# Kernel optimization log

Hardware: AMD Instinct MI355X
Metric: run time of the kernel (lower is better)

## Reference

```python
import jax, jax.numpy as jnp
import numpy as np

D_MODEL = 32
N_HEADS = 8
QUERY_SHAPE = 24
MEM_FLANGE = 8


def conv2d(x, w, padding=1):
    return jax.lax.conv_general_dilated(
        x, w, window_strides=(1, 1),
        padding=[(padding, padding), (padding, padding)],
        dimension_numbers=('NCHW', 'OIHW', 'NCHW'))


def setup_inputs() -> dict:
    key = jax.random.key(0)
    k1, k2, k3, k4 = jax.random.split(key, 4)
    x = jax.random.normal(k1, (2, 32, 32, 480), dtype=jnp.float32)
    qkv_w = jax.random.normal(k2, (96, 32, 3, 3), dtype=jnp.float32) * 0.05
    qkv_b = jax.random.normal(k3, (96,), dtype=jnp.float32) * 0.05
    out_w = jax.random.normal(k4, (32, 32, 3, 3), dtype=jnp.float32) * 0.05
    return {'x': x, 'qkv_w': qkv_w, 'qkv_b': qkv_b, 'out_w': out_w}


def reference(x, qkv_w, qkv_b, out_w):
    qs, mf, nh = QUERY_SHAPE, MEM_FLANGE, N_HEADS
    dh = D_MODEL // nh  # depth per head

    qkv = conv2d(x, qkv_w) + qkv_b[None, :, None, None]  # [B, 3*d_model, H, W0]
    # pad time (last dim) to multiple of query_shape
    W0 = qkv.shape[-1]
    off = (-W0) % qs
    if off > 0:
        qkv = jnp.pad(qkv, ((0, 0), (0, 0), (0, 0), (0, off)))
    B, _, H, W = qkv.shape

    qkv = qkv.reshape(B, nh, 3 * dh, H, W)
    q, k, v = jnp.split(qkv, 3, axis=2)  # each [B, nh, dh, H, W]
    q = q * dh ** (-0.5)
    k = jnp.pad(k, ((0, 0),) * 4 + ((mf, mf),))
    v = jnp.pad(v, ((0, 0),) * 4 + ((mf, mf),))

    nb = W // qs            # number of time blocks
    wlen = qs + 2 * mf      # key window length
    # overlapping window gather indices: [nb, wlen]
    idx = jnp.arange(nb)[:, None] * qs + jnp.arange(wlen)[None, :]

    qb = q.reshape(B, nh, dh, H, nb, qs)      # [B,nh,dh,H,nb,qs]
    kb = k[..., idx]                          # [B,nh,dh,H,nb,wlen]
    vb = v[..., idx]                          # [B,nh,dh,H,nb,wlen]

    # flatten to per-block matmuls, matching torch permutes/reshapes
    qm = qb.transpose(0, 1, 4, 3, 5, 2).reshape(-1, H * qs, dh)        # [BN, H*qs, dh]
    km = kb.transpose(0, 1, 4, 2, 3, 5).reshape(-1, dh, H * wlen)      # [BN, dh, H*wlen]
    vm = vb.transpose(0, 1, 4, 3, 5, 2).reshape(-1, H * wlen, dh)      # [BN, H*wlen, dh]

    bias = (jnp.abs(km).sum(axis=-2, keepdims=True) == 0).astype(km.dtype) * (-1e-09)
    logits = qm @ km + bias                    # [BN, H*qs, H*wlen]
    weights = jax.nn.softmax(logits, axis=-1)
    out = weights @ vm                         # [BN, H*qs, dh]

    out = out.reshape(B, nh, nb, H, qs, dh)
    out = out.transpose(0, 1, 5, 3, 2, 4)      # [B, nh, dh, H, nb, qs]
    out = out.reshape(B, nh * dh, H, nb * qs)  # [B, d_model, H, W]
    out = out[..., :x.shape[2], :x.shape[3]]
    return conv2d(out, out_w)
```

## Files before the change

kernel.cpp:

```cpp
#include <hip/hip_runtime.h>
#include <hip/hip_bf16.h>


#define HW 15360
#define VSTRIDE 1300

typedef _Float16 half4 __attribute__((ext_vector_type(4)));
typedef float floatx4 __attribute__((ext_vector_type(4)));
using fh2 = decltype(__builtin_amdgcn_cvt_pkrtz(0.f, 0.f));

__global__ __launch_bounds__(256) void repack_gemm(
    const float* __restrict__ w1, uint2* __restrict__ wA1,
    const float* __restrict__ w2, uint2* __restrict__ wA2) {
    int i = blockIdx.x * 256 + threadIdx.x;
    const float* src; uint2* dst; int rel;
    if (i < 6 * 18 * 64)            { src = w1; dst = wA1; rel = i; }
    else if (i < (6 + 2) * 18 * 64) { src = w2; dst = wA2; rel = i - 6 * 18 * 64; }
    else return;
    int lane = rel & 63;
    int mk   = rel >> 6;
    int kt   = mk % 18;
    int m    = mk / 18;
    int co   = m * 16 + (lane & 15);
    int k0   = kt * 16 + (lane >> 4) * 4;
    float v[4];
#pragma unroll
    for (int j = 0; j < 4; ++j) {
        int k = k0 + j, tap = k >> 5, ci = k & 31;
        v[j] = src[co * 288 + ci * 9 + tap];
    }
    unsigned lo = __builtin_bit_cast(unsigned, __builtin_amdgcn_cvt_pkrtz(v[0], v[1]));
    unsigned hi = __builtin_bit_cast(unsigned, __builtin_amdgcn_cvt_pkrtz(v[2], v[3]));
    dst[mk * 64 + lane] = make_uint2(lo, hi);
}

__global__ __launch_bounds__(256) void conv1_gemm(
    const float* __restrict__ x, const uint2* __restrict__ wA,
    const float* __restrict__ bias, _Float16* __restrict__ qkv)
{
    __shared__ _Float16 S[6 * 18 * 36];

    int xb  = blockIdx.x;
    int byq = blockIdx.y;
    int mb  = blockIdx.z;
    int yq = byq & 7, b = byq >> 3;
    int y0 = yq * 4, x0 = xb * 16;
    int tid = threadIdx.x, lane = tid & 63, wv = tid >> 6;

    const float* xb_ = x + (size_t)b * 32 * HW;
    for (int e = tid; e < 3456; e += 256) {
        int col = e % 18; int t2 = e / 18; int row = t2 % 6; int ci = t2 / 6;
        int yg = y0 + row - 1, xg = x0 + col - 1;
        _Float16 v = (_Float16)0.f;
        if ((unsigned)yg < 32u && (unsigned)xg < 480u)
            v = (_Float16)xb_[ci * HW + yg * 480 + xg];
        S[(row * 18 + col) * 36 + ci] = v;
    }
    __syncthreads();

    int cb = lane & 15, kg = lane >> 4;

    half4 Bf[18];
#pragma unroll
    for (int kt = 0; kt < 18; ++kt) {
        int tap = kt >> 1;
        int dy = tap / 3, dx = tap % 3;
        int ci0 = (kt & 1) * 16 + kg * 4;
        Bf[kt] = *(const half4*)&S[((wv + dy) * 18 + cb + dx) * 36 + ci0];
    }

    floatx4 acc[3];
#pragma unroll
    for (int m = 0; m < 3; ++m) {
        const float4 bz = *(const float4*)&bias[(mb * 3 + m) * 16 + kg * 4];
        acc[m] = floatx4{ bz.x, bz.y, bz.z, bz.w };
    }

    for (int kt = 0; kt < 18; ++kt) {
        half4 bb = Bf[kt];
#pragma unroll
        for (int m = 0; m < 3; ++m) {
            uint2 aw = wA[((mb * 3 + m) * 18 + kt) * 64 + lane];
            acc[m] = __builtin_amdgcn_mfma_f32_16x16x16f16(
                __builtin_bit_cast(half4, aw), bb, acc[m], 0, 0, 0);
        }
    }

    size_t obase = (size_t)b * 96 * HW + (y0 + wv) * 480 + x0 + cb;
#pragma unroll
    for (int m = 0; m < 3; ++m)
#pragma unroll
        for (int r = 0; r < 4; ++r)
            qkv[obase + (size_t)((mb * 3 + m) * 16 + kg * 4 + r) * HW] =
                (_Float16)acc[m][r];
}

__global__ __launch_bounds__(256) void conv2_gemm(
    const _Float16* __restrict__ att, const uint2* __restrict__ wA,
    float* __restrict__ out)
{
    int xb  = blockIdx.x;
    int byq = blockIdx.y;
    int yq = byq & 7, b = byq >> 3;
    int y0 = yq * 4, x0 = xb * 16;
    int tid = threadIdx.x, lane = tid & 63, wv = tid >> 6;
    int cb = lane & 15, kg = lane >> 4;
    int yrow = y0 + wv;

    const _Float16* ab = att + (size_t)b * 15360 * 32;
    const half4 hz = { (_Float16)0.f, (_Float16)0.f, (_Float16)0.f, (_Float16)0.f };

    half4 Bf[18];
#pragma unroll
    for (int kt = 0; kt < 18; ++kt) {
        int tap = kt >> 1;
        int dy = tap / 3 - 1, dx = tap % 3 - 1;
        int ci0 = (kt & 1) * 16 + kg * 4;
        int yg = yrow + dy, xg = x0 + cb + dx;
        bool ok = ((unsigned)yg < 32u) & ((unsigned)xg < 480u);
        int yc = ok ? yg : 0, xc = ok ? xg : 0;
        half4 v = *(const half4*)&ab[((size_t)yc * 480 + xc) * 32 + ci0];
        Bf[kt] = ok ? v : hz;
    }

    floatx4 acc[2];
    acc[0] = floatx4{0.f, 0.f, 0.f, 0.f};
    acc[1] = floatx4{0.f, 0.f, 0.f, 0.f};

    for (int kt = 0; kt < 18; ++kt) {
        half4 bb = Bf[kt];
#pragma unroll
        for (int m = 0; m < 2; ++m) {
            uint2 aw = wA[(m * 18 + kt) * 64 + lane];
            acc[m] = __builtin_amdgcn_mfma_f32_16x16x16f16(
                __builtin_bit_cast(half4, aw), bb, acc[m], 0, 0, 0);
        }
    }

    size_t obase = (size_t)b * 32 * HW + yrow * 480 + x0 + cb;
#pragma unroll
    for (int m = 0; m < 2; ++m)
#pragma unroll
        for (int r = 0; r < 4; ++r)
            out[obase + (size_t)(m * 16 + kg * 4 + r) * HW] = acc[m][r];
}

__global__ __launch_bounds__(256) void attn_mfma(
    const _Float16* __restrict__ qkv, _Float16* __restrict__ att)
{
    __shared__ _Float16 Kl[1280 * 4];
    __shared__ _Float16 Vl[5 * VSTRIDE];
    __shared__ _Float16 Zl[8];

    int wg    = blockIdx.x;
    int orig  = (wg & 7) * 160 + (wg >> 3);
    int qg    = orig & 3;
    int bhblk = orig >> 2;
    int blk = bhblk % 20;
    int h   = (bhblk / 20) % 8;
    int b   = bhblk / 160;
    int tid  = threadIdx.x;
    int lane = tid & 63;
    int wv   = tid >> 6;

    const _Float16* base = qkv + (size_t)(b * 96 + h * 12) * HW;
    const _Float16* kb = base + 4 * HW;
    const _Float16* vb = base + 8 * HW;

    const _Float16 h0 = (_Float16)0.f;
    if (tid < 2) *(half4*)&Zl[tid * 4] = half4{ h0, h0, h0, h0 };

    for (int j = tid; j < 1280; j += 256) {
        int yy = j / 40, wc = j - yy * 40;
        int wpos = blk * 24 + wc - 8;
        _Float16 k0 = h0, k1 = h0, k2 = h0, k3 = h0;
        _Float16 v0 = h0, v1 = h0, v2 = h0, v3 = h0;
        if ((unsigned)wpos < 480u) {
            int o = yy * 480 + wpos;
            k0 = kb[o]; k1 = kb[o + HW]; k2 = kb[o + 2 * HW]; k3 = kb[o + 3 * HW];
            v0 = vb[o]; v1 = vb[o + HW]; v2 = vb[o + 2 * HW]; v3 = vb[o + 3 * HW];
        }
        *(half4*)&Kl[j * 4] = half4{ k0, k1, k2, k3 };
        Vl[j]               = v0;
        Vl[VSTRIDE + j]     = v1;
        Vl[2 * VSTRIDE + j] = v2;
        Vl[3 * VSTRIDE + j] = v3;
        Vl[4 * VSTRIDE + j] = (_Float16)1.0f;
    }

    const float QS = 0.5f * 1.44269504f;
    half4 qf[3];
#pragma unroll
    for (int t = 0; t < 3; ++t) {
        half4 qq = { h0, h0, h0, h0 };
        if (lane < 16) {
            int q = qg * 192 + (wv * 3 + t) * 16 + lane;
            int y = q / 24, qc = q - y * 24;
            int o = y * 480 + blk * 24 + qc;
            qq[0] = (_Float16)((float)base[o] * QS);
            qq[1] = (_Float16)((float)base[o + HW] * QS);
            qq[2] = (_Float16)((float)base[o + 2 * HW] * QS);
            qq[3] = (_Float16)((float)base[o + 3 * HW] * QS);
        }
        qf[t] = qq;
    }

    __syncthreads();

    const floatx4 fz = { 0.f, 0.f, 0.f, 0.f };
    floatx4 acc[3];
#pragma unroll
    for (int t = 0; t < 3; ++t) acc[t] = fz;

    int n = lane & 15;
    int g = lane >> 4;

    const _Float16* kap = (lane < 16) ? &Kl[n * 4] : Zl;
    int kstep = (lane < 16) ? 64 : 0;
    const _Float16* vap = (n <= 4) ? &Vl[n * VSTRIDE + g * 4] : Zl;
    int vstep = (n <= 4) ? 16 : 0;

    for (int kt = 0; kt < 80; ++kt) {
        half4 ka = *(const half4*)kap; kap += kstep;
        half4 vv = *(const half4*)vap; vap += vstep;
#pragma unroll
        for (int t = 0; t < 3; ++t) {
            floatx4 s = __builtin_amdgcn_mfma_f32_16x16x16f16(ka, qf[t], fz, 0, 0, 0);
            auto lo = __builtin_amdgcn_cvt_pkrtz(__builtin_amdgcn_exp2f(s[0]),
                                                 __builtin_amdgcn_exp2f(s[1]));
            auto hi = __builtin_amdgcn_cvt_pkrtz(__builtin_amdgcn_exp2f(s[2]),
                                                 __builtin_amdgcn_exp2f(s[3]));
            half4 pa = { (_Float16)lo[0], (_Float16)lo[1],
                         (_Float16)hi[0], (_Float16)hi[1] };
            acc[t] = __builtin_amdgcn_mfma_f32_16x16x16f16(pa, vv, acc[t], 0, 0, 0);
        }
    }

#pragma unroll
    for (int t = 0; t < 3; ++t) {
#pragma unroll
        for (int r = 0; r < 4; ++r) {
            float ls = __shfl(acc[t][r], (lane & 48) + 4);
            if (n < 4) {
                float val = acc[t][r] * __builtin_amdgcn_rcpf(ls);
                int q = qg * 192 + (wv * 3 + t) * 16 + g * 4 + r;
                int y = q / 24, qc = q - y * 24;
                att[((size_t)b * 15360 + y * 480 + blk * 24 + qc) * 32 + h * 4 + n] =
                    (_Float16)val;
            }
        }
    }
}

extern "C" void kernel_launch(void* const* d_in, const int* in_sizes, int n_in,
                              void* d_out, int out_size, void* d_ws, size_t ws_size,
                              hipStream_t stream) {
    const float* x     = (const float*)d_in[0];
    const float* qkv_w = (const float*)d_in[1];
    const float* qkv_b = (const float*)d_in[2];
    const float* out_w = (const float*)d_in[3];
    float* out = (float*)d_out;

    uint2* wA1 = (uint2*)d_ws;
    uint2* wA2 = wA1 + 6 * 18 * 64;
    _Float16* qkv16 = (_Float16*)(wA2 + 2 * 18 * 64);
    _Float16* att16 = qkv16 + (size_t)2 * 96 * HW;

    repack_gemm<<<(8 * 18 * 64 + 255) / 256, 256, 0, stream>>>(
        qkv_w, wA1, out_w, wA2);

    conv1_gemm<<<dim3(30, 16, 2), 256, 0, stream>>>(x, wA1, qkv_b, qkv16);

    attn_mfma<<<1280, 256, 0, stream>>>(qkv16, att16);

    conv2_gemm<<<dim3(30, 16), 256, 0, stream>>>(att16, wA2, out);
}
```

Before: 78.62 us.

## Store QKV intermediate channel-last so conv1 and attention use vector accesses

The fp16 QKV intermediate moves from a channel-planar layout [B,96,H,W] to a pixel-major, channel-last layout [B,H,W,96]. Conv1 now writes four adjacent channels with one half4 store instead of four scalar strided stores. The attention kernel loads each K, V and Q head slice as one 8-byte half4 per pixel instead of four scalar loads spaced HW apart. In exchange, neighbouring threads now access memory 192 bytes apart, which may coalesce less well than the old contiguous-per-channel accesses.

```diff
diff --git a/kernel.cpp b/kernel.cpp
--- a/kernel.cpp
+++ b/kernel.cpp
@@ -86,13 +86,13 @@
         }
     }
 
-    size_t obase = (size_t)b * 96 * HW + (y0 + wv) * 480 + x0 + cb;
-#pragma unroll
-    for (int m = 0; m < 3; ++m)
-#pragma unroll
-        for (int r = 0; r < 4; ++r)
-            qkv[obase + (size_t)((mb * 3 + m) * 16 + kg * 4 + r) * HW] =
-                (_Float16)acc[m][r];
+    size_t pbase = ((size_t)b * HW + (y0 + wv) * 480 + x0 + cb) * 96;
+#pragma unroll
+    for (int m = 0; m < 3; ++m) {
+        half4 hv = { (_Float16)acc[m][0], (_Float16)acc[m][1],
+                     (_Float16)acc[m][2], (_Float16)acc[m][3] };
+        *(half4*)&qkv[pbase + (mb * 3 + m) * 16 + kg * 4] = hv;
+    }
 }
 
 __global__ __launch_bounds__(256) void conv2_gemm(
@@ -107,7 +107,7 @@
     int cb = lane & 15, kg = lane >> 4;
     int yrow = y0 + wv;
 
-    const _Float16* ab = att + (size_t)b * 15360 * 32;
+    const _Float16* ab = att + (size_t)b * HW * 32;
     const half4 hz = { (_Float16)0.f, (_Float16)0.f, (_Float16)0.f, (_Float16)0.f };
 
     half4 Bf[18];
@@ -163,28 +163,26 @@
     int lane = tid & 63;
     int wv   = tid >> 6;
 
-    const _Float16* base = qkv + (size_t)(b * 96 + h * 12) * HW;
-    const _Float16* kb = base + 4 * HW;
-    const _Float16* vb = base + 8 * HW;
+    const _Float16* base = qkv + (size_t)b * HW * 96 + h * 12;
 
     const _Float16 h0 = (_Float16)0.f;
-    if (tid < 2) *(half4*)&Zl[tid * 4] = half4{ h0, h0, h0, h0 };
+    const half4 hz4 = { h0, h0, h0, h0 };
+    if (tid < 2) *(half4*)&Zl[tid * 4] = hz4;
 
     for (int j = tid; j < 1280; j += 256) {
         int yy = j / 40, wc = j - yy * 40;
         int wpos = blk * 24 + wc - 8;
-        _Float16 k0 = h0, k1 = h0, k2 = h0, k3 = h0;
-        _Float16 v0 = h0, v1 = h0, v2 = h0, v3 = h0;
+        half4 k4 = hz4, v4 = hz4;
         if ((unsigned)wpos < 480u) {
-            int o = yy * 480 + wpos;
-            k0 = kb[o]; k1 = kb[o + HW]; k2 = kb[o + 2 * HW]; k3 = kb[o + 3 * HW];
-            v0 = vb[o]; v1 = vb[o + HW]; v2 = vb[o + 2 * HW]; v3 = vb[o + 3 * HW];
-        }
-        *(half4*)&Kl[j * 4] = half4{ k0, k1, k2, k3 };
-        Vl[j]               = v0;
-        Vl[VSTRIDE + j]     = v1;
-        Vl[2 * VSTRIDE + j] = v2;
-        Vl[3 * VSTRIDE + j] = v3;
+            size_t o = (size_t)(yy * 480 + wpos) * 96;
+            k4 = *(const half4*)&base[o + 4];
+            v4 = *(const half4*)&base[o + 8];
+        }
+        *(half4*)&Kl[j * 4] = k4;
+        Vl[j]               = v4[0];
+        Vl[VSTRIDE + j]     = v4[1];
+        Vl[2 * VSTRIDE + j] = v4[2];
+        Vl[3 * VSTRIDE + j] = v4[3];
         Vl[4 * VSTRIDE + j] = (_Float16)1.0f;
     }
 
@@ -192,15 +190,16 @@
     half4 qf[3];
 #pragma unroll
     for (int t = 0; t < 3; ++t) {
-        half4 qq = { h0, h0, h0, h0 };
+        half4 qq = hz4;
         if (lane < 16) {
             int q = qg * 192 + (wv * 3 + t) * 16 + lane;
             int y = q / 24, qc = q - y * 24;
-            int o = y * 480 + blk * 24 + qc;
-            qq[0] = (_Float16)((float)base[o] * QS);
-            qq[1] = (_Float16)((float)base[o + HW] * QS);
-            qq[2] = (_Float16)((float)base[o + 2 * HW] * QS);
-            qq[3] = (_Float16)((float)base[o + 3 * HW] * QS);
+            size_t o = (size_t)(y * 480 + blk * 24 + qc) * 96;
+            half4 qv = *(const half4*)&base[o];
+            qq[0] = (_Float16)((float)qv[0] * QS);
+            qq[1] = (_Float16)((float)qv[1] * QS);
+            qq[2] = (_Float16)((float)qv[2] * QS);
+            qq[3] = (_Float16)((float)qv[3] * QS);
         }
         qf[t] = qq;
     }
@@ -245,7 +244,7 @@
                 float val = acc[t][r] * __builtin_amdgcn_rcpf(ls);
                 int q = qg * 192 + (wv * 3 + t) * 16 + g * 4 + r;
                 int y = q / 24, qc = q - y * 24;
-                att[((size_t)b * 15360 + y * 480 + blk * 24 + qc) * 32 + h * 4 + n] =
+                att[((size_t)b * HW + y * 480 + blk * 24 + qc) * 32 + h * 4 + n] =
                     (_Float16)val;
             }
         }
@@ -264,7 +263,7 @@
     uint2* wA1 = (uint2*)d_ws;
     uint2* wA2 = wA1 + 6 * 18 * 64;
     _Float16* qkv16 = (_Float16*)(wA2 + 2 * 18 * 64);
-    _Float16* att16 = qkv16 + (size_t)2 * 96 * HW;
+    _Float16* att16 = qkv16 + (size_t)2 * HW * 96;
 
     repack_gemm<<<(8 * 18 * 64 + 255) / 256, 256, 0, stream>>>(
         qkv_w, wA1, out_w, wA2);
```

New measurement: 85.69 us. +9.0%, slower.
